# Kernel optimization log

Measured on AMD Instinct MI355X. Metric: run time of the kernel, lower is better.

## Reference

```python
import jax, jax.numpy as jnp
import numpy as np

ALPHA, GAMMA = 0.25, 2.0
IOU_THRES = 0.5
WEIGHTS = (10.0, 10.0, 5.0, 5.0, 15.0)
MAXV = 16  # max polygon verts during quad-vs-quad clipping (<=8, padded)


def box_corners(b):
    # b: (5,) = cx, cy, w, h, theta(rad); returns (4,2) CCW corners
    cx, cy, w, h, t = b[0], b[1], b[2], b[3], b[4]
    c, s = jnp.cos(t), jnp.sin(t)
    dx = jnp.array([-0.5, 0.5, 0.5, -0.5]) * w
    dy = jnp.array([-0.5, -0.5, 0.5, 0.5]) * h
    return jnp.stack([cx + dx * c - dy * s, cy + dx * s + dy * c], axis=-1)


def pair_iou(b1, b2):
    # exact rotated-rectangle IoU via Sutherland-Hodgman clipping
    p1 = box_corners(b1)
    p2 = box_corners(b2)
    poly = jnp.zeros((MAXV, 2)).at[:4].set(p1)
    n = jnp.int32(4)
    for e in range(4):
        a = p2[e]
        d = p2[(e + 1) % 4] - a
        out = jnp.zeros((MAXV, 2))
        m = jnp.int32(0)
        for i in range(MAXV):
            cur = poly[i]
            nxt = poly[jnp.where(i + 1 >= n, 0, i + 1)]
            sc = d[0] * (cur[1] - a[1]) - d[1] * (cur[0] - a[0])
            sn = d[0] * (nxt[1] - a[1]) - d[1] * (nxt[0] - a[0])
            valid = i < n
            keep = valid & (sc >= 0)
            out = out.at[m].set(jnp.where(keep, cur, out[m]))
            m = m + keep.astype(jnp.int32)
            crossed = valid & ((sc >= 0) != (sn >= 0))
            den = sc - sn
            t = sc / jnp.where(den == 0, 1.0, den)
            ip = cur + t * (nxt - cur)
            out = out.at[m].set(jnp.where(crossed, ip, out[m]))
            m = m + crossed.astype(jnp.int32)
        poly, n = out, m
    idx = jnp.arange(MAXV)
    nxt = jnp.where(idx + 1 >= n, 0, idx + 1)
    cr = poly[:, 0] * poly[nxt, 1] - poly[nxt, 0] * poly[:, 1]
    inter = 0.5 * jnp.abs(jnp.sum(jnp.where(idx < n, cr, 0.0)))
    union = b1[2] * b1[3] + b2[2] * b2[3] - inter
    return inter / jnp.maximum(union, 1e-9)


rbox_iou_mat = jax.vmap(jax.vmap(pair_iou, (None, 0)), (0, None))  # (A,5),(G,5)->(A,G)


def min_area_square(rb):
    s = jnp.maximum(rb[:, 2], rb[:, 3])
    return jnp.stack([rb[:, 0] - s / 2, rb[:, 1] - s / 2,
                      rb[:, 0] + s / 2, rb[:, 1] + s / 2], 1)


def bbox_overlaps(a, b):
    lt = jnp.maximum(a[:, None, :2], b[None, :, :2])
    rb = jnp.minimum(a[:, None, 2:], b[None, :, 2:])
    wh = jnp.clip(rb - lt, 0.0)
    inter = wh[..., 0] * wh[..., 1]
    aa = (a[:, 2] - a[:, 0]) * (a[:, 3] - a[:, 1])
    ab = (b[:, 2] - b[:, 0]) * (b[:, 3] - b[:, 1])
    return inter / jnp.maximum(aa[:, None] + ab[None, :] - inter, 1e-9)


def encode(ex, gt):
    wx, wy, ww, wh, wt = WEIGHTS
    ew = jnp.maximum(ex[:, 2], 1.0); eh = jnp.maximum(ex[:, 3], 1.0)
    gw = jnp.maximum(gt[:, 2], 1.0); gh = jnp.maximum(gt[:, 3], 1.0)
    dx = wx * (gt[:, 0] - ex[:, 0]) / ew
    dy = wy * (gt[:, 1] - ex[:, 1]) / eh
    dw = ww * jnp.log(gw / ew)
    dh = wh * jnp.log(gh / eh)
    dt = wt * (jnp.tan(gt[:, 4]) - jnp.tan(ex[:, 4]))
    return jnp.stack([dx, dy, dw, dh, dt], 1)


def lmr5pangle(anch, dt):
    # encoded angle offset of the 90-degree-swapped box: tan(t+pi/2) = -1/tan(t)
    wt = WEIGHTS[4]
    ta = jnp.tan(anch[:, 4])
    tg = dt / wt + ta
    tg = jnp.where(jnp.abs(tg) < 1e-4, jnp.where(tg < 0, -1e-4, 1e-4), tg)
    return wt * (-1.0 / tg - ta)


def landmark_encode(ex, lm):
    wx, wy = WEIGHTS[0], WEIGHTS[1]
    ew = jnp.maximum(ex[:, 2], 1.0); eh = jnp.maximum(ex[:, 3], 1.0)
    return jnp.stack([wx * (lm[:, 0] - ex[:, 0]) / ew,
                      wy * (lm[:, 1] - ex[:, 1]) / eh,
                      wx * (lm[:, 2] - ex[:, 0]) / ew,
                      wy * (lm[:, 3] - ex[:, 1]) / eh], 1)


def smooth_l1(d, beta=1.0 / 9):
    d = jnp.abs(d)
    return jnp.where(d < beta, 0.5 * d * d / beta, d - 0.5 * beta)


def lmr5p_per_anchor(pred, tgt, anch):
    t22 = lmr5pangle(anch, pred[:, 4])
    l1 = smooth_l1(tgt[:, 0] - pred[:, 0])
    l2 = smooth_l1(tgt[:, 1] - pred[:, 1])
    l3 = smooth_l1(tgt[:, 2] - pred[:, 2])
    l4 = smooth_l1(tgt[:, 3] - pred[:, 3])
    l5 = smooth_l1(tgt[:, 2] - pred[:, 3])  # |w1 - h2|
    l6 = smooth_l1(tgt[:, 3] - pred[:, 2])  # |h1 - w2|
    l7 = smooth_l1(tgt[:, 4] - pred[:, 4])
    l8 = smooth_l1(tgt[:, 4] - t22)
    return jnp.minimum(l1 + l2 + l3 + l4 + l7, l1 + l2 + l5 + l6 + l8)


def balanced_l1(d, beta=0.5, al=0.5, ga=0.9):
    d = jnp.abs(d)
    b = np.e ** (ga / al) - 1.0
    return jnp.where(d < beta,
                     al / b * (b * d + 1.0) * jnp.log(b * d / beta + 1.0) - al * d,
                     ga * d + ga / b - al * beta)


def per_image(cls, reg, lmk, anch, ann, ls):
    valid_g = ann[:, -1] != -1.0
    has_gt = jnp.any(valid_g)
    cls = jnp.clip(cls, 1e-4, 1.0 - 1e-4)
    indicator = bbox_overlaps(min_area_square(anch), min_area_square(ann[:, :5]))
    riou = rbox_iou_mat(anch, ann[:, :5])
    ious = jnp.where(indicator >= 0.1, riou, 0.0)   # rbox_overlaps thresh=0.1 gating
    ious = jnp.where(valid_g[None, :], ious, -1.0)  # mask padded gts
    ious = jax.lax.stop_gradient(ious)              # torch computes ious on cpu numpy
    iou_max = ious.max(1)
    iou_argmax = ious.argmax(1)
    pos = iou_max >= IOU_THRES
    max_gt = ious.max(0)
    argmax_gt = ious.argmax(0)
    force = valid_g & (max_gt < IOU_THRES)
    pos = (pos.astype(jnp.int32).at[argmax_gt].max(force.astype(jnp.int32))) > 0
    num_pos = pos.sum()
    denom = jnp.maximum(num_pos.astype(cls.dtype), 1.0)
    assigned = ann[iou_argmax]                       # (A, 6)
    lab = assigned[:, -1].astype(jnp.int32)
    onehot = (lab[:, None] == jnp.arange(cls.shape[-1])[None, :]).astype(cls.dtype)
    tgt = jnp.where(pos[:, None], onehot,
                    jnp.where((iou_max < IOU_THRES - 0.1)[:, None], 0.0, -1.0))
    af = jnp.where(tgt == 1.0, ALPHA, 1.0 - ALPHA)
    fw = af * jnp.where(tgt == 1.0, 1.0 - cls, cls) ** GAMMA
    bce = -(tgt * jnp.log(cls + 1e-6) + (1.0 - tgt) * jnp.log(1.0 - cls + 1e-6))
    cls_loss = jnp.where(tgt != -1.0, fw * bce, 0.0).sum() / denom
    cls_loss = jnp.where(has_gt, cls_loss, 0.0)
    gt_safe = jnp.where(pos[:, None], assigned[:, :5], anch)  # keep masked lanes finite
    tg1 = encode(anch, gt_safe)
    r1 = jnp.where(pos, lmr5p_per_anchor(reg, tg1, anch), 0.0).sum() / (5.0 * denom)
    r1 = jnp.where(has_gt & (num_pos > 0), r1, 0.0)
    lm_safe = jnp.where(pos[:, None], ls[iou_argmax],
                        jnp.stack([anch[:, 0], anch[:, 1], anch[:, 0], anch[:, 1]], 1))
    tg2 = landmark_encode(anch, lm_safe)
    r2 = jnp.where(pos[:, None], balanced_l1(lmk - tg2), 0.0).sum() / (4.0 * denom)
    r2 = jnp.where(has_gt & (num_pos > 0), r2, 0.0)
    return cls_loss, r1, r2


def setup_inputs() -> dict:
    B, A, G, C = 2, 16384, 24, 8
    NV = 16  # valid gts per image; remaining rows padded with label -1
    ks = jax.random.split(jax.random.key(0), 16)
    classifications = jax.random.uniform(ks[0], (B, A, C), jnp.float32)
    regressions = jax.random.normal(ks[1], (B, A, 5), jnp.float32) * 0.1
    landmarks = jax.random.normal(ks[2], (B, A, 4), jnp.float32) * 0.1
    gcx = 100.0 + 800.0 * jax.random.uniform(ks[3], (B, G))
    gcy = 100.0 + 800.0 * jax.random.uniform(ks[4], (B, G))
    gw = 40.0 + 160.0 * jax.random.uniform(ks[5], (B, G))
    gh = 40.0 + 160.0 * jax.random.uniform(ks[6], (B, G))
    gth = 1.2 * jax.random.uniform(ks[7], (B, G)) - 0.6
    lab = jax.random.randint(ks[8], (B, G), 0, C).astype(jnp.float32)
    lab = jnp.where(jnp.arange(G)[None, :] >= NV, -1.0, lab)
    annotations = jnp.stack([gcx, gcy, gw, gh, gth, lab], -1)
    acx = 1024.0 * jax.random.uniform(ks[9], (B, A))
    acy = 1024.0 * jax.random.uniform(ks[10], (B, A))
    aw = 16.0 + 112.0 * jax.random.uniform(ks[11], (B, A))
    ah = 16.0 + 112.0 * jax.random.uniform(ks[12], (B, A))
    ath = 1.2 * jax.random.uniform(ks[13], (B, A)) - 0.6
    anchors = jnp.stack([acx, acy, aw, ah, ath], -1)
    # plant jittered copies of the gts so a healthy number of anchors are positive
    jit = jax.random.normal(ks[14], (B, G, 5)) * jnp.array([2.0, 2.0, 2.0, 2.0, 0.01])
    anchors = anchors.at[:, :G, :].set(annotations[:, :, :5] + jit)
    ca, sa = jnp.cos(gth), jnp.sin(gth)
    gt_linestrips = jnp.stack([gcx - 0.4 * gw * ca, gcy - 0.4 * gw * sa,
                               gcx + 0.4 * gw * ca, gcy + 0.4 * gw * sa], -1)
    return {"classifications": classifications, "regressions": regressions,
            "anchors": anchors, "annotations": annotations,
            "landmarks": landmarks, "gt_linestrips": gt_linestrips}


def reference(classifications, regressions, anchors, annotations, landmarks, gt_linestrips):
    cls_l, r1, r2 = jax.vmap(per_image)(classifications, regressions, landmarks,
                                        anchors, annotations, gt_linestrips)
    return (cls_l.mean(keepdims=True), r1.mean(keepdims=True), r2.mean(keepdims=True))
```

## Files before the change

kernel.cpp:

```cpp
#include <hip/hip_runtime.h>
#include <math.h>

#define B_N 2
#define A_N 16384
#define G_N 24
#define C_N 8
#define NV8 8
#define BPI 256
#define RECL 33

#define OFF_GCOL   0
#define OFF_AKEY   (512 * G_N * 8)
#define OFF_PART   (OFF_AKEY + B_N * A_N * 8)

__device__ inline unsigned int fmap(float v) {
    unsigned int u = __float_as_uint(v);
    return (u & 0x80000000u) ? ~u : (u | 0x80000000u);
}
__device__ inline float funmap(unsigned int u) {
    unsigned int bits = (u & 0x80000000u) ? (u ^ 0x80000000u) : ~u;
    return __uint_as_float(bits);
}
__device__ inline unsigned long long mkkey(float v, int idx) {
    return ((unsigned long long)fmap(v) << 32) |
           (unsigned long long)(0xFFFFFFFFu - (unsigned int)idx);
}
__device__ inline float key_val(unsigned long long k) { return funmap((unsigned int)(k >> 32)); }
__device__ inline int   key_idx(unsigned long long k) { return (int)(0xFFFFFFFFu - (unsigned int)k); }

__device__ inline float smoothl1(float x) {
    const float beta = 1.0f / 9.0f;
    float d = fabsf(x);
    return (d < beta) ? (0.5f * d * d / beta) : (d - 0.5f * beta);
}
__device__ inline float balancedl1(float x) {
    const float bb  = 5.049647464412945f;
    const float alb = 0.5f / 5.049647464412945f;
    const float gab = 0.9f / 5.049647464412945f;
    float d = fabsf(x);
    if (d < 0.5f)
        return alb * (bb * d + 1.0f) * logf(bb * d / 0.5f + 1.0f) - 0.5f * d;
    return 0.9f * d + gab - 0.25f;
}
__device__ inline float focal_pos(const float* cr, int lab) {
    float s = 0.0f;
#pragma unroll
    for (int c = 0; c < C_N; c++) {
        float p = fminf(fmaxf(cr[c], 1e-4f), 0.9999f);
        if (c == lab) s += 0.25f * (1.0f - p) * (1.0f - p) * (-logf(p + 1e-6f));
        else          s += 0.75f * p * p * (-logf(1.0f - p + 1e-6f));
    }
    return s;
}
__device__ inline float focal_neg(const float* cr) {
    float s = 0.0f;
#pragma unroll
    for (int c = 0; c < C_N; c++) {
        float p = fminf(fmaxf(cr[c], 1e-4f), 0.9999f);
        s += 0.75f * p * p * (-logf(1.0f - p + 1e-6f));
    }
    return s;
}
__device__ inline float reg_loss_v(const float* rr, float acx, float acy, float aw,
                                   float ah, float ath, const float* gl) {
    float aw1 = fmaxf(aw, 1.0f), ah1 = fmaxf(ah, 1.0f);
    float gw1 = fmaxf(gl[16], 1.0f), gh1 = fmaxf(gl[17], 1.0f);
    float t1 = 10.0f * (gl[14] - acx) / aw1;
    float t2 = 10.0f * (gl[15] - acy) / ah1;
    float t3 = 5.0f * logf(gw1 / aw1);
    float t4 = 5.0f * logf(gh1 / ah1);
    float ta = tanf(ath);
    float t5 = 15.0f * (gl[20] - ta);
    float p0 = rr[0], p1 = rr[1], p2 = rr[2], p3 = rr[3], p4 = rr[4];
    float tg = p4 / 15.0f + ta;
    if (fabsf(tg) < 1e-4f) tg = (tg < 0.0f) ? -1e-4f : 1e-4f;
    float t22 = 15.0f * (-1.0f / tg - ta);
    float l1 = smoothl1(t1 - p0), l2 = smoothl1(t2 - p1);
    float l3 = smoothl1(t3 - p2), l4 = smoothl1(t4 - p3);
    float l5 = smoothl1(t3 - p3), l6 = smoothl1(t4 - p2);
    float l7 = smoothl1(t5 - p4), l8 = smoothl1(t5 - t22);
    return fminf(l1 + l2 + l3 + l4 + l7, l1 + l2 + l5 + l6 + l8);
}
__device__ inline float lmk_loss_v(const float* lk, float acx, float acy, float aw,
                                   float ah, const float* gl) {
    float aw1 = fmaxf(aw, 1.0f), ah1 = fmaxf(ah, 1.0f);
    return balancedl1(lk[0] - 10.0f * (gl[21] - acx) / aw1)
         + balancedl1(lk[1] - 10.0f * (gl[22] - acy) / ah1)
         + balancedl1(lk[2] - 10.0f * (gl[23] - acx) / aw1)
         + balancedl1(lk[3] - 10.0f * (gl[24] - acy) / ah1);
}
__device__ inline float reg_loss(const float* rr, const float* ar, const float* annr) {
    float acx = ar[0], acy = ar[1], aw = ar[2], ah = ar[3], ath = ar[4];
    float aw1 = fmaxf(aw, 1.0f), ah1 = fmaxf(ah, 1.0f);
    float gw1 = fmaxf(annr[2], 1.0f), gh1 = fmaxf(annr[3], 1.0f);
    float t1 = 10.0f * (annr[0] - acx) / aw1;
    float t2 = 10.0f * (annr[1] - acy) / ah1;
    float t3 = 5.0f * logf(gw1 / aw1);
    float t4 = 5.0f * logf(gh1 / ah1);
    float ta = tanf(ath);
    float t5 = 15.0f * (tanf(annr[4]) - ta);
    float p0 = rr[0], p1 = rr[1], p2 = rr[2], p3 = rr[3], p4 = rr[4];
    float tg = p4 / 15.0f + ta;
    if (fabsf(tg) < 1e-4f) tg = (tg < 0.0f) ? -1e-4f : 1e-4f;
    float t22 = 15.0f * (-1.0f / tg - ta);
    float l1 = smoothl1(t1 - p0), l2 = smoothl1(t2 - p1);
    float l3 = smoothl1(t3 - p2), l4 = smoothl1(t4 - p3);
    float l5 = smoothl1(t3 - p3), l6 = smoothl1(t4 - p2);
    float l7 = smoothl1(t5 - p4), l8 = smoothl1(t5 - t22);
    return fminf(l1 + l2 + l3 + l4 + l7, l1 + l2 + l5 + l6 + l8);
}
__device__ inline float lmk_loss(const float* lk, const float* ar, const float* lr) {
    float acx = ar[0], acy = ar[1];
    float aw1 = fmaxf(ar[2], 1.0f), ah1 = fmaxf(ar[3], 1.0f);
    return balancedl1(lk[0] - 10.0f * (lr[0] - acx) / aw1)
         + balancedl1(lk[1] - 10.0f * (lr[1] - acy) / ah1)
         + balancedl1(lk[2] - 10.0f * (lr[2] - acx) / aw1)
         + balancedl1(lk[3] - 10.0f * (lr[3] - acy) / ah1);
}

__global__ __launch_bounds__(64) void k_main(
    const float* __restrict__ cls, const float* __restrict__ reg,
    const float* __restrict__ anch, const float* __restrict__ ann,
    const float* __restrict__ lmk, const float* __restrict__ ls,
    unsigned long long* __restrict__ gcol, unsigned long long* __restrict__ akey,
    float* __restrict__ partials)
{
    __shared__ float  glds[G_N * RECL];
    __shared__ float2 pb2[2 * NV8 * 64];
    __shared__ float  acor[9][64];
    __shared__ unsigned long long rowk[64];
    __shared__ unsigned long long colk[G_N];
    __shared__ unsigned short wl[G_N * 64];

    const int tid = threadIdx.x;
    const int b   = blockIdx.x >> 8;
    const int a   = ((blockIdx.x & (BPI - 1)) << 6) | tid;
    const size_t idx = (size_t)b * A_N + a;

    const float* ar = anch + idx * 5;
    float acx = ar[0], acy = ar[1], aw = ar[2], ah = ar[3], ath = ar[4];
    float4 c0 = ((const float4*)cls)[idx * 2];
    float4 c1 = ((const float4*)cls)[idx * 2 + 1];
    const float* rr = reg + idx * 5;
    float rv[5] = {rr[0], rr[1], rr[2], rr[3], rr[4]};
    float4 lv = ((const float4*)lmk)[idx];
    float an0 = 0, an1 = 0, an2 = 0, an3 = 0, an4 = 0, an5 = -1.0f;
    float ls0 = 0, ls1 = 0, ls2 = 0, ls3 = 0;
    if (tid < G_N) {
        const float* annr = ann + (size_t)(b * G_N + tid) * 6;
        an0 = annr[0]; an1 = annr[1]; an2 = annr[2];
        an3 = annr[3]; an4 = annr[4]; an5 = annr[5];
        const float* lr = ls + (size_t)(b * G_N + tid) * 4;
        ls0 = lr[0]; ls1 = lr[1]; ls2 = lr[2]; ls3 = lr[3];
    }
    float crv[C_N] = {c0.x, c0.y, c0.z, c0.w, c1.x, c1.y, c1.z, c1.w};

    if (tid < G_N) {
        float* r = glds + tid * RECL;
        float c2 = cosf(an4), s2 = sinf(an4);
        const float dxs[4] = {-0.5f, 0.5f, 0.5f, -0.5f};
        const float dys[4] = {-0.5f, -0.5f, 0.5f, 0.5f};
#pragma unroll
        for (int k = 0; k < 4; k++) {
            float ex = dxs[k] * an2, ey = dys[k] * an3;
            r[k]     = an0 + ex * c2 - ey * s2;
            r[4 + k] = an1 + ex * s2 + ey * c2;
        }
        r[8] = an2 * an3;
        float sg = fmaxf(an2, an3);
        float gx1 = an0 - sg * 0.5f, gy1 = an1 - sg * 0.5f;
        float gx2 = an0 + sg * 0.5f, gy2 = an1 + sg * 0.5f;
        r[9] = gx1; r[10] = gy1; r[11] = gx2; r[12] = gy2;
        r[13] = (gx2 - gx1) * (gy2 - gy1);
        r[14] = an0; r[15] = an1; r[16] = an2; r[17] = an3; r[18] = an4; r[19] = an5;
        r[20] = tanf(an4);
        r[21] = ls0; r[22] = ls1; r[23] = ls2; r[24] = ls3;
        colk[tid] = 0ull;
    }
    unsigned int validmask =
        (unsigned int)__ballot(tid < G_N && an5 != -1.0f);
    int first_valid = validmask ? (__ffs((int)validmask) - 1) : -1;
    rowk[tid] = (first_valid >= 0) ? mkkey(0.0f, first_valid) : 0ull;

    {
        float c1_ = cosf(ath), s1_ = sinf(ath);
        const float dxs[4] = {-0.5f, 0.5f, 0.5f, -0.5f};
        const float dys[4] = {-0.5f, -0.5f, 0.5f, 0.5f};
#pragma unroll
        for (int k = 0; k < 4; k++) {
            float dx = dxs[k] * aw, dy = dys[k] * ah;
            acor[k][tid]     = acx + dx * c1_ - dy * s1_;
            acor[4 + k][tid] = acy + dx * s1_ + dy * c1_;
        }
        acor[8][tid] = aw * ah;
    }
    __syncthreads();

    float sa = fmaxf(aw, ah);
    float ax1 = acx - sa * 0.5f, ay1 = acy - sa * 0.5f;
    float ax2 = acx + sa * 0.5f, ay2 = acy + sa * 0.5f;
    float areaA = (ax2 - ax1) * (ay2 - ay1);

    int cnt = 0;
    for (unsigned int vm = validmask; vm; vm &= vm - 1) {
        int g = __ffs((int)vm) - 1;
        const float* gq = glds + g * RECL;
        float iw = fmaxf(fminf(ax2, gq[11]) - fmaxf(ax1, gq[9]), 0.0f);
        float ih = fmaxf(fminf(ay2, gq[12]) - fmaxf(ay1, gq[10]), 0.0f);
        float inter0 = iw * ih;
        float ind = inter0 / fmaxf(areaA + gq[13] - inter0, 1e-9f);
        bool pass = (ind >= 0.1f);
        unsigned long long bal = __ballot(pass);
        if (pass) {
            int off = __popcll(bal & ((1ull << tid) - 1ull));
            wl[cnt + off] = (unsigned short)((tid << 5) | g);
        }
        cnt += __popcll(bal);
    }
    __syncthreads();

    for (int i = tid; i < cnt; i += 64) {
        unsigned int e = wl[i];
        int owner = (int)(e >> 5);
        int g = (int)(e & 31u);
        const float* gl = glds + g * RECL;
        float p2x[4], p2y[4];
#pragma unroll
        for (int k = 0; k < 4; k++) { p2x[k] = gl[k]; p2y[k] = gl[4 + k]; }
        float ax_[4], ay_[4];
#pragma unroll
        for (int k = 0; k < 4; k++) { ax_[k] = acor[k][owner]; ay_[k] = acor[4 + k][owner]; }

        int n;
        {
            float apx = p2x[0], apy = p2y[0];
            float dxe = p2x[1] - apx, dye = p2y[1] - apy;
            int m = 0;
#pragma unroll
            for (int v = 0; v < 4; v++) {
                float cx_ = ax_[v], cy_ = ay_[v];
                float nx_ = ax_[(v + 1) & 3], ny_ = ay_[(v + 1) & 3];
                float sc = dxe * (cy_ - apy) - dye * (cx_ - apx);
                float sn = dxe * (ny_ - apy) - dye * (nx_ - apx);
                bool ci = (sc >= 0.0f), niv = (sn >= 0.0f);
                if (ci) {
                    if (m < NV8) pb2[(0 * NV8 + m) * 64 + tid] = make_float2(cx_, cy_);
                    m++;
                }
                if (ci != niv) {
                    float den = sc - sn;
                    float t = sc / ((den == 0.0f) ? 1.0f : den);
                    if (m < NV8) pb2[(0 * NV8 + m) * 64 + tid] =
                        make_float2(cx_ + t * (nx_ - cx_), cy_ + t * (ny_ - cy_));
                    m++;
                }
            }
            n = m;
        }
        for (int eidx = 1; eidx <= 2; eidx++) {
            int src = (eidx == 1) ? 0 : 1;
            int dst = (eidx == 1) ? 1 : 0;
            float apx = p2x[eidx], apy = p2y[eidx];
            float dxe = p2x[(eidx + 1) & 3] - apx, dye = p2y[(eidx + 1) & 3] - apy;
            int m = 0;
            if (n > 0) {
                float2 first = pb2[(src * NV8 + 0) * 64 + tid];
                float2 cur = first;
                float2 pref = (n > 1) ? pb2[(src * NV8 + 1) * 64 + tid] : first;
                for (int v = 0; v < n; v++) {
                    float2 nxt = (v + 1 < n) ? pref : first;
                    if (v + 2 < n) pref = pb2[(src * NV8 + v + 2) * 64 + tid];
                    float sc = dxe * (cur.y - apy) - dye * (cur.x - apx);
                    float sn = dxe * (nxt.y - apy) - dye * (nxt.x - apx);
                    bool ci = (sc >= 0.0f), niv = (sn >= 0.0f);
                    if (ci) {
                        if (m < NV8) pb2[(dst * NV8 + m) * 64 + tid] = cur;
                        m++;
                    }
                    if (ci != niv) {
                        float den = sc - sn;
                        float t = sc / ((den == 0.0f) ? 1.0f : den);
                        if (m < NV8) pb2[(dst * NV8 + m) * 64 + tid] =
                            make_float2(cur.x + t * (nxt.x - cur.x), cur.y + t * (nxt.y - cur.y));
                        m++;
                    }
                    cur = nxt;
                }
            }
            n = m;
        }
        float ssum = 0.0f;
        {
            float apx = p2x[3], apy = p2y[3];
            float dxe = p2x[0] - apx, dye = p2y[0] - apy;
            float2 efirst = make_float2(0.0f, 0.0f), eprev = efirst;
            int fcnt = 0;
            if (n > 0) {
                float2 first = pb2[(0 * NV8 + 0) * 64 + tid];
                float2 cur = first;
                float2 pref = (n > 1) ? pb2[(0 * NV8 + 1) * 64 + tid] : first;
                for (int v = 0; v < n; v++) {
                    float2 nxt = (v + 1 < n) ? pref : first;
                    if (v + 2 < n) pref = pb2[(0 * NV8 + v + 2) * 64 + tid];
                    float sc = dxe * (cur.y - apy) - dye * (cur.x - apx);
                    float sn = dxe * (nxt.y - apy) - dye * (nxt.x - apx);
                    bool ci = (sc >= 0.0f), niv = (sn >= 0.0f);
                    if (ci) {
                        if (fcnt == 0) efirst = cur;
                        else ssum += eprev.x * cur.y - cur.x * eprev.y;
                        eprev = cur; fcnt++;
                    }
                    if (ci != niv) {
                        float den = sc - sn;
                        float t = sc / ((den == 0.0f) ? 1.0f : den);
                        float2 ip = make_float2(cur.x + t * (nxt.x - cur.x),
                                                cur.y + t * (nxt.y - cur.y));
                        if (fcnt == 0) efirst = ip;
                        else ssum += eprev.x * ip.y - ip.x * eprev.y;
                        eprev = ip; fcnt++;
                    }
                    cur = nxt;
                }
            }
            if (fcnt > 0) ssum += eprev.x * efirst.y - efirst.x * eprev.y;
        }
        float interA = 0.5f * fabsf(ssum);
        float uni = acor[8][owner] + gl[8] - interA;
        float val = interA / fmaxf(uni, 1e-9f);

        atomicMax(&rowk[owner], mkkey(val, g));
        if (val > 0.0f) {
            int aowner = ((blockIdx.x & (BPI - 1)) << 6) | owner;
            atomicMax(&colk[g], mkkey(val, aowner));
        }
    }
    __syncthreads();

    if (tid < G_N)
        gcol[(size_t)blockIdx.x * G_N + tid] = colk[tid];

    unsigned long long rowkey = rowk[tid];
    akey[idx] = rowkey;

    float iou_max = key_val(rowkey);
    int gmax = key_idx(rowkey);
    float cls_sum = 0.0f, reg_sum = 0.0f, lmk_sum = 0.0f;
    int pc = 0;
    if (iou_max >= 0.5f) {
        const float* gl = glds + gmax * RECL;
        pc = 1;
        cls_sum = focal_pos(crv, (int)gl[19]);
        reg_sum = reg_loss_v(rv, acx, acy, aw, ah, ath, gl);
        float lkv[4] = {lv.x, lv.y, lv.z, lv.w};
        lmk_sum = lmk_loss_v(lkv, acx, acy, aw, ah, gl);
    } else if (iou_max < 0.4f) {
        cls_sum = focal_neg(crv);
    }

    float fpc = (float)pc;
    for (int off = 32; off; off >>= 1) {
        cls_sum += __shfl_down(cls_sum, off);
        reg_sum += __shfl_down(reg_sum, off);
        lmk_sum += __shfl_down(lmk_sum, off);
        fpc     += __shfl_down(fpc, off);
    }
    if (tid == 0) {
        float* p = partials + (size_t)blockIdx.x * 4;
        p[0] = cls_sum; p[1] = reg_sum; p[2] = lmk_sum; p[3] = fpc;
    }
}

__global__ __launch_bounds__(384) void k_fix(
    const float* __restrict__ cls, const float* __restrict__ reg,
    const float* __restrict__ anch, const float* __restrict__ ann,
    const float* __restrict__ lmk, const float* __restrict__ ls,
    const unsigned long long* __restrict__ gcol, const unsigned long long* __restrict__ akey,
    const float* __restrict__ partials, float* __restrict__ out)
{
    __shared__ unsigned long long colpart[B_N * G_N * 8];
    __shared__ unsigned long long colfin[B_N * G_N];
    __shared__ float res[B_N][3];
    const int tid = threadIdx.x;
    const int b = (tid >> 6) & 1, lane = tid & 63;

    double s0 = 0.0, s1 = 0.0, s2 = 0.0, s3 = 0.0;
    if (tid < 128) {
        for (int r = lane; r < BPI; r += 64) {
            const float* p = partials + (size_t)(b * BPI + r) * 4;
            s0 += p[0]; s1 += p[1]; s2 += p[2]; s3 += p[3];
        }
        for (int off = 32; off; off >>= 1) {
            s0 += __shfl_down(s0, off);
            s1 += __shfl_down(s1, off);
            s2 += __shfl_down(s2, off);
            s3 += __shfl_down(s3, off);
        }
    }

    {
        int pair = tid >> 3, sub = tid & 7;
        int pb = pair / G_N, g = pair - pb * G_N;
        unsigned long long k = mkkey(0.0f, 0);
        for (int r = sub; r < BPI; r += 8) {
            unsigned long long v = gcol[(size_t)(pb * BPI + r) * G_N + g];
            if (v > k) k = v;
        }
        colpart[pair * 8 + sub] = k;
    }
    __syncthreads();
    if (tid < B_N * G_N) {
        unsigned long long k = colpart[tid * 8];
#pragma unroll
        for (int s = 1; s < 8; s++) {
            unsigned long long v = colpart[tid * 8 + s];
            if (v > k) k = v;
        }
        colfin[tid] = k;
    }
    __syncthreads();

    const float* annb = ann + (size_t)b * G_N * 6;
    float dc = 0.0f, dr = 0.0f, dl = 0.0f; int dn = 0;
    if (tid < 128 && lane < G_N) {
        bool valid = annb[lane * 6 + 5] != -1.0f;
        unsigned long long k = colfin[b * G_N + lane];
        int fa = key_idx(k);
        bool force = valid && (key_val(k) < 0.5f);
        if (force) {
            for (int g2 = 0; g2 < lane; g2++) {
                if (annb[g2 * 6 + 5] == -1.0f) continue;
                unsigned long long k2 = colfin[b * G_N + g2];
                if (key_val(k2) < 0.5f && key_idx(k2) == fa) { force = false; break; }
            }
        }
        if (force) {
            size_t fidx = (size_t)b * A_N + fa;
            unsigned long long ak = akey[fidx];
            float im = key_val(ak);
            if (!(im >= 0.5f)) {
                dn = 1;
                int gm = key_idx(ak);
                const float* cr = cls + fidx * C_N;
                float crv[C_N];
#pragma unroll
                for (int c = 0; c < C_N; c++) crv[c] = cr[c];
                const float* annr = annb + gm * 6;
                const float* arr = anch + fidx * 5;
                dc = focal_pos(crv, (int)annr[5]);
                if (im < 0.4f) dc -= focal_neg(crv);
                dr = reg_loss(reg + fidx * 5, arr, annr);
                dl = lmk_loss(lmk + fidx * 4, arr, ls + (size_t)(b * G_N + gm) * 4);
            }
        }
    }
    if (tid < 128) {
        float fdn = (float)dn;
        for (int off = 32; off; off >>= 1) {
            dc  += __shfl_down(dc, off);
            dr  += __shfl_down(dr, off);
            dl  += __shfl_down(dl, off);
            fdn += __shfl_down(fdn, off);
        }
        if (lane == 0) {
            bool has_gt = false;
            for (int g = 0; g < G_N; g++)
                if (annb[g * 6 + 5] != -1.0f) has_gt = true;
            float np = (float)s3 + fdn;
            float denom = fmaxf(np, 1.0f);
            res[b][0] = has_gt ? (float)((s0 + dc) / denom) : 0.0f;
            res[b][1] = (has_gt && np > 0.0f) ? (float)((s1 + dr) / (5.0 * denom)) : 0.0f;
            res[b][2] = (has_gt && np > 0.0f) ? (float)((s2 + dl) / (4.0 * denom)) : 0.0f;
        }
    }
    __syncthreads();
    if (tid == 0) {
        out[0] = (res[0][0] + res[1][0]) * 0.5f;
        out[1] = (res[0][1] + res[1][1]) * 0.5f;
        out[2] = (res[0][2] + res[1][2]) * 0.5f;
    }
}

extern "C" void kernel_launch(void* const* d_in, const int* in_sizes, int n_in,
                              void* d_out, int out_size, void* d_ws, size_t ws_size,
                              hipStream_t stream)
{
    (void)in_sizes; (void)n_in; (void)out_size; (void)ws_size;
    const float* cls  = (const float*)d_in[0];
    const float* reg  = (const float*)d_in[1];
    const float* anch = (const float*)d_in[2];
    const float* ann  = (const float*)d_in[3];
    const float* lmk  = (const float*)d_in[4];
    const float* ls   = (const float*)d_in[5];

    char* ws = (char*)d_ws;
    unsigned long long* gcol = (unsigned long long*)(ws + OFF_GCOL);
    unsigned long long* akey = (unsigned long long*)(ws + OFF_AKEY);
    float* partials = (float*)(ws + OFF_PART);
    float* out = (float*)d_out;

    hipLaunchKernelGGL(k_main, dim3(B_N * BPI), dim3(64), 0, stream,
                       cls, reg, anch, ann, lmk, ls, gcol, akey, partials);
    hipLaunchKernelGGL(k_fix, dim3(1), dim3(384), 0, stream,
                       cls, reg, anch, ann, lmk, ls, gcol, akey, partials, out);
}
```

Measured before the change: 87.81 us.

## Fuse main and fixup kernels via cooperative grid sync with 256-thread blocks

Merges the per-anchor kernel and the single-block fixup kernel into one cooperative launch that uses a grid-wide sync, which removes the second kernel launch and its gap. Blocks grow from 64 to 256 threads, each wave keeping its own worklist and column keys, so there are 128 blocks in place of 512. Cooperative launch requires every block to be resident at once, and the grid sync adds a barrier cost. The larger shared-memory footprint per block may also lower occupancy.

After: 132.8 us. +51.3%, slower.

```diff
diff --git a/kernel.cpp b/kernel.cpp
--- a/kernel.cpp
+++ b/kernel.cpp
@@ -1,12 +1,17 @@
 #include <hip/hip_runtime.h>
+#include <hip/hip_cooperative_groups.h>
 #include <math.h>
+
+namespace cg = cooperative_groups;
 
 #define B_N 2
 #define A_N 16384
 #define G_N 24
 #define C_N 8
 #define NV8 8
-#define BPI 256
+#define TPB 256
+#define BLKS (B_N * A_N / TPB)
+#define WPI  (A_N / 64)
 #define RECL 33
 
 #define OFF_GCOL   0
@@ -118,23 +123,29 @@
          + balancedl1(lk[3] - 10.0f * (lr[3] - acy) / ah1);
 }
 
-__global__ __launch_bounds__(64) void k_main(
+__global__ __launch_bounds__(TPB) void k_all(
     const float* __restrict__ cls, const float* __restrict__ reg,
     const float* __restrict__ anch, const float* __restrict__ ann,
     const float* __restrict__ lmk, const float* __restrict__ ls,
     unsigned long long* __restrict__ gcol, unsigned long long* __restrict__ akey,
-    float* __restrict__ partials)
+    float* __restrict__ partials, float* __restrict__ out)
 {
     __shared__ float  glds[G_N * RECL];
-    __shared__ float2 pb2[2 * NV8 * 64];
-    __shared__ float  acor[9][64];
-    __shared__ unsigned long long rowk[64];
-    __shared__ unsigned long long colk[G_N];
-    __shared__ unsigned short wl[G_N * 64];
-
-    const int tid = threadIdx.x;
-    const int b   = blockIdx.x >> 8;
-    const int a   = ((blockIdx.x & (BPI - 1)) << 6) | tid;
+    __shared__ float2 pb2[2 * NV8 * TPB];
+    __shared__ float  acor[9][TPB];
+    __shared__ unsigned long long rowk[TPB];
+    __shared__ unsigned long long colk[4][G_N];
+    __shared__ unsigned short wl[4][G_N * 64];
+    __shared__ unsigned long long colpart[48 * 4];
+    __shared__ unsigned long long colfin[48];
+    __shared__ float res[B_N][3];
+
+    const int tid  = threadIdx.x;
+    const int w    = tid >> 6, lane = tid & 63;
+    const int b    = blockIdx.x >> 6;
+    const int blk  = blockIdx.x & 63;
+    const int wgi  = blk * 4 + w;
+    const int a    = wgi * 64 + lane;
     const size_t idx = (size_t)b * A_N + a;
 
     const float* ar = anch + idx * 5;
@@ -144,18 +155,13 @@
     const float* rr = reg + idx * 5;
     float rv[5] = {rr[0], rr[1], rr[2], rr[3], rr[4]};
     float4 lv = ((const float4*)lmk)[idx];
-    float an0 = 0, an1 = 0, an2 = 0, an3 = 0, an4 = 0, an5 = -1.0f;
-    float ls0 = 0, ls1 = 0, ls2 = 0, ls3 = 0;
+    float crv[C_N] = {c0.x, c0.y, c0.z, c0.w, c1.x, c1.y, c1.z, c1.w};
+
     if (tid < G_N) {
         const float* annr = ann + (size_t)(b * G_N + tid) * 6;
-        an0 = annr[0]; an1 = annr[1]; an2 = annr[2];
-        an3 = annr[3]; an4 = annr[4]; an5 = annr[5];
+        float an0 = annr[0], an1 = annr[1], an2 = annr[2];
+        float an3 = annr[3], an4 = annr[4], an5 = annr[5];
         const float* lr = ls + (size_t)(b * G_N + tid) * 4;
-        ls0 = lr[0]; ls1 = lr[1]; ls2 = lr[2]; ls3 = lr[3];
-    }
-    float crv[C_N] = {c0.x, c0.y, c0.z, c0.w, c1.x, c1.y, c1.z, c1.w};
-
-    if (tid < G_N) {
         float* r = glds + tid * RECL;
         float c2 = cosf(an4), s2 = sinf(an4);
         const float dxs[4] = {-0.5f, 0.5f, 0.5f, -0.5f};
@@ -174,13 +180,9 @@
         r[13] = (gx2 - gx1) * (gy2 - gy1);
         r[14] = an0; r[15] = an1; r[16] = an2; r[17] = an3; r[18] = an4; r[19] = an5;
         r[20] = tanf(an4);
-        r[21] = ls0; r[22] = ls1; r[23] = ls2; r[24] = ls3;
-        colk[tid] = 0ull;
-    }
-    unsigned int validmask =
-        (unsigned int)__ballot(tid < G_N && an5 != -1.0f);
-    int first_valid = validmask ? (__ffs((int)validmask) - 1) : -1;
-    rowk[tid] = (first_valid >= 0) ? mkkey(0.0f, first_valid) : 0ull;
+        r[21] = lr[0]; r[22] = lr[1]; r[23] = lr[2]; r[24] = lr[3];
+    }
+    if (lane < G_N) colk[w][lane] = 0ull;
 
     {
         float c1_ = cosf(ath), s1_ = sinf(ath);
@@ -195,6 +197,15 @@
         acor[8][tid] = aw * ah;
     }
     __syncthreads();
+
+    unsigned int validmask = 0; int first_valid = -1;
+    for (int g = 0; g < G_N; g++) {
+        if (glds[g * RECL + 19] != -1.0f) {
+            validmask |= (1u << g);
+            if (first_valid < 0) first_valid = g;
+        }
+    }
+    rowk[tid] = (first_valid >= 0) ? mkkey(0.0f, first_valid) : 0ull;
 
     float sa = fmaxf(aw, ah);
     float ax1 = acx - sa * 0.5f, ay1 = acy - sa * 0.5f;
@@ -212,24 +223,24 @@
         bool pass = (ind >= 0.1f);
         unsigned long long bal = __ballot(pass);
         if (pass) {
-            int off = __popcll(bal & ((1ull << tid) - 1ull));
-            wl[cnt + off] = (unsigned short)((tid << 5) | g);
+            int off = __popcll(bal & ((1ull << lane) - 1ull));
+            wl[w][cnt + off] = (unsigned short)((lane << 5) | g);
         }
         cnt += __popcll(bal);
     }
-    __syncthreads();
-
-    for (int i = tid; i < cnt; i += 64) {
-        unsigned int e = wl[i];
+
+    for (int i = lane; i < cnt; i += 64) {
+        unsigned int e = wl[w][i];
         int owner = (int)(e >> 5);
         int g = (int)(e & 31u);
+        int ot = (w << 6) | owner;
         const float* gl = glds + g * RECL;
         float p2x[4], p2y[4];
 #pragma unroll
         for (int k = 0; k < 4; k++) { p2x[k] = gl[k]; p2y[k] = gl[4 + k]; }
         float ax_[4], ay_[4];
 #pragma unroll
-        for (int k = 0; k < 4; k++) { ax_[k] = acor[k][owner]; ay_[k] = acor[4 + k][owner]; }
+        for (int k = 0; k < 4; k++) { ax_[k] = acor[k][ot]; ay_[k] = acor[4 + k][ot]; }
 
         int n;
         {
@@ -244,13 +255,13 @@
                 float sn = dxe * (ny_ - apy) - dye * (nx_ - apx);
                 bool ci = (sc >= 0.0f), niv = (sn >= 0.0f);
                 if (ci) {
-                    if (m < NV8) pb2[(0 * NV8 + m) * 64 + tid] = make_float2(cx_, cy_);
+                    if (m < NV8) pb2[(0 * NV8 + m) * TPB + tid] = make_float2(cx_, cy_);
                     m++;
                 }
                 if (ci != niv) {
                     float den = sc - sn;
                     float t = sc / ((den == 0.0f) ? 1.0f : den);
-                    if (m < NV8) pb2[(0 * NV8 + m) * 64 + tid] =
+                    if (m < NV8) pb2[(0 * NV8 + m) * TPB + tid] =
                         make_float2(cx_ + t * (nx_ - cx_), cy_ + t * (ny_ - cy_));
                     m++;
                 }
@@ -264,23 +275,23 @@
             float dxe = p2x[(eidx + 1) & 3] - apx, dye = p2y[(eidx + 1) & 3] - apy;
             int m = 0;
             if (n > 0) {
-                float2 first = pb2[(src * NV8 + 0) * 64 + tid];
+                float2 first = pb2[(src * NV8 + 0) * TPB + tid];
                 float2 cur = first;
-                float2 pref = (n > 1) ? pb2[(src * NV8 + 1) * 64 + tid] : first;
+                float2 pref = (n > 1) ? pb2[(src * NV8 + 1) * TPB + tid] : first;
                 for (int v = 0; v < n; v++) {
                     float2 nxt = (v + 1 < n) ? pref : first;
-                    if (v + 2 < n) pref = pb2[(src * NV8 + v + 2) * 64 + tid];
+                    if (v + 2 < n) pref = pb2[(src * NV8 + v + 2) * TPB + tid];
                     float sc = dxe * (cur.y - apy) - dye * (cur.x - apx);
                     float sn = dxe * (nxt.y - apy) - dye * (nxt.x - apx);
                     bool ci = (sc >= 0.0f), niv = (sn >= 0.0f);
                     if (ci) {
-                        if (m < NV8) pb2[(dst * NV8 + m) * 64 + tid] = cur;
+                        if (m < NV8) pb2[(dst * NV8 + m) * TPB + tid] = cur;
                         m++;
                     }
                     if (ci != niv) {
                         float den = sc - sn;
                         float t = sc / ((den == 0.0f) ? 1.0f : den);
-                        if (m < NV8) pb2[(dst * NV8 + m) * 64 + tid] =
+                        if (m < NV8) pb2[(dst * NV8 + m) * TPB + tid] =
                             make_float2(cur.x + t * (nxt.x - cur.x), cur.y + t * (nxt.y - cur.y));
                         m++;
                     }
@@ -296,12 +307,12 @@
             float2 efirst = make_float2(0.0f, 0.0f), eprev = efirst;
             int fcnt = 0;
             if (n > 0) {
-                float2 first = pb2[(0 * NV8 + 0) * 64 + tid];
+                float2 first = pb2[(0 * NV8 + 0) * TPB + tid];
                 float2 cur = first;
-                float2 pref = (n > 1) ? pb2[(0 * NV8 + 1) * 64 + tid] : first;
+                float2 pref = (n > 1) ? pb2[(0 * NV8 + 1) * TPB + tid] : first;
                 for (int v = 0; v < n; v++) {
                     float2 nxt = (v + 1 < n) ? pref : first;
-                    if (v + 2 < n) pref = pb2[(0 * NV8 + v + 2) * 64 + tid];
+                    if (v + 2 < n) pref = pb2[(0 * NV8 + v + 2) * TPB + tid];
                     float sc = dxe * (cur.y - apy) - dye * (cur.x - apx);
                     float sn = dxe * (nxt.y - apy) - dye * (nxt.x - apx);
                     bool ci = (sc >= 0.0f), niv = (sn >= 0.0f);
@@ -325,19 +336,18 @@
             if (fcnt > 0) ssum += eprev.x * efirst.y - efirst.x * eprev.y;
         }
         float interA = 0.5f * fabsf(ssum);
-        float uni = acor[8][owner] + gl[8] - interA;
+        float uni = acor[8][ot] + gl[8] - interA;
         float val = interA / fmaxf(uni, 1e-9f);
 
-        atomicMax(&rowk[owner], mkkey(val, g));
+        atomicMax(&rowk[ot], mkkey(val, g));
         if (val > 0.0f) {
-            int aowner = ((blockIdx.x & (BPI - 1)) << 6) | owner;
-            atomicMax(&colk[g], mkkey(val, aowner));
-        }
-    }
-    __syncthreads();
-
-    if (tid < G_N)
-        gcol[(size_t)blockIdx.x * G_N + tid] = colk[tid];
+            int aowner = wgi * 64 + owner;
+            atomicMax(&colk[w][g], mkkey(val, aowner));
+        }
+    }
+
+    if (lane < G_N)
+        gcol[(size_t)(b * WPI + wgi) * G_N + lane] = colk[w][lane];
 
     unsigned long long rowkey = rowk[tid];
     akey[idx] = rowkey;
@@ -364,29 +374,21 @@
         lmk_sum += __shfl_down(lmk_sum, off);
         fpc     += __shfl_down(fpc, off);
     }
-    if (tid == 0) {
-        float* p = partials + (size_t)blockIdx.x * 4;
+    if (lane == 0) {
+        float* p = partials + (size_t)(b * WPI + wgi) * 4;
         p[0] = cls_sum; p[1] = reg_sum; p[2] = lmk_sum; p[3] = fpc;
     }
-}
-
-__global__ __launch_bounds__(384) void k_fix(
-    const float* __restrict__ cls, const float* __restrict__ reg,
-    const float* __restrict__ anch, const float* __restrict__ ann,
-    const float* __restrict__ lmk, const float* __restrict__ ls,
-    const unsigned long long* __restrict__ gcol, const unsigned long long* __restrict__ akey,
-    const float* __restrict__ partials, float* __restrict__ out)
-{
-    __shared__ unsigned long long colpart[B_N * G_N * 8];
-    __shared__ unsigned long long colfin[B_N * G_N];
-    __shared__ float res[B_N][3];
-    const int tid = threadIdx.x;
-    const int b = (tid >> 6) & 1, lane = tid & 63;
+
+    __threadfence();
+    cg::this_grid().sync();
+    if (blockIdx.x != 0) return;
+
+    const int b2 = (tid >> 6) & 1, lane2 = tid & 63;
 
     double s0 = 0.0, s1 = 0.0, s2 = 0.0, s3 = 0.0;
     if (tid < 128) {
-        for (int r = lane; r < BPI; r += 64) {
-            const float* p = partials + (size_t)(b * BPI + r) * 4;
+        for (int r = lane2; r < WPI; r += 64) {
+            const float* p = partials + (size_t)(b2 * WPI + r) * 4;
             s0 += p[0]; s1 += p[1]; s2 += p[2]; s3 += p[3];
         }
         for (int off = 32; off; off >>= 1) {
@@ -398,58 +400,60 @@
     }
 
     {
-        int pair = tid >> 3, sub = tid & 7;
-        int pb = pair / G_N, g = pair - pb * G_N;
-        unsigned long long k = mkkey(0.0f, 0);
-        for (int r = sub; r < BPI; r += 8) {
-            unsigned long long v = gcol[(size_t)(pb * BPI + r) * G_N + g];
-            if (v > k) k = v;
-        }
-        colpart[pair * 8 + sub] = k;
+        int pair = tid >> 2, sub = tid & 3;
+        if (pair < B_N * G_N) {
+            int pb_ = pair / G_N, g = pair - pb_ * G_N;
+            unsigned long long k = mkkey(0.0f, 0);
+            for (int r = sub; r < WPI; r += 4) {
+                unsigned long long v = gcol[(size_t)(pb_ * WPI + r) * G_N + g];
+                if (v > k) k = v;
+            }
+            colpart[pair * 4 + sub] = k;
+        }
     }
     __syncthreads();
     if (tid < B_N * G_N) {
-        unsigned long long k = colpart[tid * 8];
-#pragma unroll
-        for (int s = 1; s < 8; s++) {
-            unsigned long long v = colpart[tid * 8 + s];
+        unsigned long long k = colpart[tid * 4];
+#pragma unroll
+        for (int s = 1; s < 4; s++) {
+            unsigned long long v = colpart[tid * 4 + s];
             if (v > k) k = v;
         }
         colfin[tid] = k;
     }
     __syncthreads();
 
-    const float* annb = ann + (size_t)b * G_N * 6;
+    const float* annb = ann + (size_t)b2 * G_N * 6;
     float dc = 0.0f, dr = 0.0f, dl = 0.0f; int dn = 0;
-    if (tid < 128 && lane < G_N) {
-        bool valid = annb[lane * 6 + 5] != -1.0f;
-        unsigned long long k = colfin[b * G_N + lane];
+    if (tid < 128 && lane2 < G_N) {
+        bool valid = annb[lane2 * 6 + 5] != -1.0f;
+        unsigned long long k = colfin[b2 * G_N + lane2];
         int fa = key_idx(k);
         bool force = valid && (key_val(k) < 0.5f);
         if (force) {
-            for (int g2 = 0; g2 < lane; g2++) {
+            for (int g2 = 0; g2 < lane2; g2++) {
                 if (annb[g2 * 6 + 5] == -1.0f) continue;
-                unsigned long long k2 = colfin[b * G_N + g2];
+                unsigned long long k2 = colfin[b2 * G_N + g2];
                 if (key_val(k2) < 0.5f && key_idx(k2) == fa) { force = false; break; }
             }
         }
         if (force) {
-            size_t fidx = (size_t)b * A_N + fa;
+            size_t fidx = (size_t)b2 * A_N + fa;
             unsigned long long ak = akey[fidx];
             float im = key_val(ak);
             if (!(im >= 0.5f)) {
                 dn = 1;
                 int gm = key_idx(ak);
                 const float* cr = cls + fidx * C_N;
-                float crv[C_N];
-#pragma unroll
-                for (int c = 0; c < C_N; c++) crv[c] = cr[c];
+                float crv2[C_N];
+#pragma unroll
+                for (int c = 0; c < C_N; c++) crv2[c] = cr[c];
                 const float* annr = annb + gm * 6;
                 const float* arr = anch + fidx * 5;
-                dc = focal_pos(crv, (int)annr[5]);
-                if (im < 0.4f) dc -= focal_neg(crv);
+                dc = focal_pos(crv2, (int)annr[5]);
+                if (im < 0.4f) dc -= focal_neg(crv2);
                 dr = reg_loss(reg + fidx * 5, arr, annr);
-                dl = lmk_loss(lmk + fidx * 4, arr, ls + (size_t)(b * G_N + gm) * 4);
+                dl = lmk_loss(lmk + fidx * 4, arr, ls + (size_t)(b2 * G_N + gm) * 4);
             }
         }
     }
@@ -461,15 +465,15 @@
             dl  += __shfl_down(dl, off);
             fdn += __shfl_down(fdn, off);
         }
-        if (lane == 0) {
+        if (lane2 == 0) {
             bool has_gt = false;
             for (int g = 0; g < G_N; g++)
                 if (annb[g * 6 + 5] != -1.0f) has_gt = true;
             float np = (float)s3 + fdn;
             float denom = fmaxf(np, 1.0f);
-            res[b][0] = has_gt ? (float)((s0 + dc) / denom) : 0.0f;
-            res[b][1] = (has_gt && np > 0.0f) ? (float)((s1 + dr) / (5.0 * denom)) : 0.0f;
-            res[b][2] = (has_gt && np > 0.0f) ? (float)((s2 + dl) / (4.0 * denom)) : 0.0f;
+            res[b2][0] = has_gt ? (float)((s0 + dc) / denom) : 0.0f;
+            res[b2][1] = (has_gt && np > 0.0f) ? (float)((s1 + dr) / (5.0 * denom)) : 0.0f;
+            res[b2][2] = (has_gt && np > 0.0f) ? (float)((s2 + dl) / (4.0 * denom)) : 0.0f;
         }
     }
     __syncthreads();
@@ -498,8 +502,8 @@
     float* partials = (float*)(ws + OFF_PART);
     float* out = (float*)d_out;
 
-    hipLaunchKernelGGL(k_main, dim3(B_N * BPI), dim3(64), 0, stream,
-                       cls, reg, anch, ann, lmk, ls, gcol, akey, partials);
-    hipLaunchKernelGGL(k_fix, dim3(1), dim3(384), 0, stream,
-                       cls, reg, anch, ann, lmk, ls, gcol, akey, partials, out);
-}
+    void* args[] = {(void*)&cls, (void*)&reg, (void*)&anch, (void*)&ann,
+                    (void*)&lmk, (void*)&ls, (void*)&gcol, (void*)&akey,
+                    (void*)&partials, (void*)&out};
+    hipLaunchCooperativeKernel((void*)k_all, dim3(BLKS), dim3(TPB), args, 0, stream);
+}
```
